# Kernel tuning notes

Measured on AMD Instinct MI355X. Metric: run time of the kernel, lower is better.

The kernel has to match this reference:

```python
import jax, jax.numpy as jnp
import numpy as np

DT = 1.0  # module init dt

def setup_inputs() -> dict:
    key = jax.random.key(0)
    k1, k2 = jax.random.split(key)
    x = jax.random.normal(k1, (8, 4096, 512), dtype=jnp.float32)
    w = jax.random.normal(k2, (512,), dtype=jnp.float32)
    return {"x": x, "w": w}

def reference(x, w):
    # h_t = h_{t-1} + dt*(x_t - relu(w)*h_{t-1}) = a*h_{t-1} + dt*x_t,  a = 1 - dt*relu(w)
    a = (1.0 - DT * jax.nn.relu(w)).astype(x.dtype)  # [d]
    h0 = jnp.zeros((x.shape[0], x.shape[2]), dtype=x.dtype)  # [b, d]
    xt = jnp.swapaxes(x, 0, 1)  # [t, b, d]

    def step(h, x_t):
        h_next = a * h + DT * x_t
        return h_next, h_next

    _, hs = jax.lax.scan(step, h0, xt)  # [t, b, d]
    return jnp.swapaxes(hs, 0, 1)  # [b, t, d] (return_sequences=True)
```

## Files before the change

kernel.cpp:

```cpp
#include <hip/hip_runtime.h>


#define RB 8
#define RT 4096
#define RD 512
#define RC 256
#define RL 16
#define DG (RD / 4)

#define HB 1e15f

__device__ __forceinline__ float sclamp(float v) {
    return fminf(fmaxf(v, -HB), HB);
}

__global__ void __launch_bounds__(DG)
k_carry(const float4* __restrict__ x4, const float4* __restrict__ w4,
        float4* __restrict__ Lc) {
    const int g  = threadIdx.x;
    const int bc = blockIdx.x;
    const int b  = bc >> 8;
    const int c  = bc & (RC - 1);

    const float4 wv = w4[g];
    const float ax = 1.0f - fmaxf(wv.x, 0.0f);
    const float ay = 1.0f - fmaxf(wv.y, 0.0f);
    const float az = 1.0f - fmaxf(wv.z, 0.0f);
    const float aw = 1.0f - fmaxf(wv.w, 0.0f);

    const float4* __restrict__ xp = x4 + ((size_t)b * RT + (size_t)c * RL) * DG + g;

    float hx = 0.f, hy = 0.f, hz = 0.f, hw = 0.f;
#pragma unroll
    for (int i = 0; i < RL; ++i) {
        const float4 v = xp[(size_t)i * DG];
        hx = sclamp(ax * hx + v.x);
        hy = sclamp(ay * hy + v.y);
        hz = sclamp(az * hz + v.z);
        hw = sclamp(aw * hw + v.w);
    }
    Lc[(size_t)bc * DG + g] = make_float4(hx, hy, hz, hw);
}

__global__ void __launch_bounds__(DG)
k_final(const float4* __restrict__ x4, const float4* __restrict__ w4,
        const float4* __restrict__ Lc, float4* __restrict__ out4) {
    const int g  = threadIdx.x;
    const int bc = blockIdx.x;
    const int b  = bc >> 8;
    const int c  = bc & (RC - 1);

    const float4 wv = w4[g];
    const float ax = 1.0f - fmaxf(wv.x, 0.0f);
    const float ay = 1.0f - fmaxf(wv.y, 0.0f);
    const float az = 1.0f - fmaxf(wv.z, 0.0f);
    const float aw = 1.0f - fmaxf(wv.w, 0.0f);

    float Ax = ax, Ay = ay, Az = az, Aw = aw;
#pragma unroll
    for (int i = 0; i < 4; ++i) {
        Ax = sclamp(Ax * Ax); Ay = sclamp(Ay * Ay);
        Az = sclamp(Az * Az); Aw = sclamp(Aw * Aw);
    }

    const float4* __restrict__ lp = Lc + (size_t)b * RC * DG + g;
    float hx = 0.f, hy = 0.f, hz = 0.f, hw = 0.f;
#pragma unroll 4
    for (int j = 0; j < c; ++j) {
        const float4 L = lp[(size_t)j * DG];
        hx = sclamp(Ax * hx + L.x);
        hy = sclamp(Ay * hy + L.y);
        hz = sclamp(Az * hz + L.z);
        hw = sclamp(Aw * hw + L.w);
    }

    const float4* __restrict__ xp = x4   + ((size_t)b * RT + (size_t)c * RL) * DG + g;
    float4*       __restrict__ op = out4 + ((size_t)b * RT + (size_t)c * RL) * DG + g;
#pragma unroll
    for (int i = 0; i < RL; ++i) {
        const float4 v = xp[(size_t)i * DG];
        hx = sclamp(ax * hx + v.x);
        hy = sclamp(ay * hy + v.y);
        hz = sclamp(az * hz + v.z);
        hw = sclamp(aw * hw + v.w);
        op[(size_t)i * DG] = make_float4(hx, hy, hz, hw);
    }
}

__global__ void __launch_bounds__(256)
rnn_seq_sat(const float* __restrict__ x, const float* __restrict__ w,
            float* __restrict__ out) {
    const int idx = blockIdx.x * blockDim.x + threadIdx.x;
    if (idx >= RB * RD) return;
    const int b = idx >> 9;
    const int d = idx & (RD - 1);
    const float a = 1.0f - fmaxf(w[d], 0.0f);
    const float* xp = x + (size_t)b * RT * RD + d;
    float* op = out + (size_t)b * RT * RD + d;
    float h = 0.f;
#pragma unroll 4
    for (int t = 0; t < RT; ++t) {
        h = sclamp(a * h + xp[(size_t)t * RD]);
        op[(size_t)t * RD] = h;
    }
}

extern "C" void kernel_launch(void* const* d_in, const int* in_sizes, int n_in,
                              void* d_out, int out_size, void* d_ws, size_t ws_size,
                              hipStream_t stream) {
    const float* x = (const float*)d_in[0];
    const float* w = (const float*)d_in[1];
    float* out = (float*)d_out;

    const size_t need = (size_t)RB * RC * DG * sizeof(float4);
    if (ws_size >= need) {
        const float4* x4 = (const float4*)x;
        const float4* w4 = (const float4*)w;
        float4* Lc = (float4*)d_ws;
        k_carry<<<dim3(RB * RC), dim3(DG), 0, stream>>>(x4, w4, Lc);
        k_final<<<dim3(RB * RC), dim3(DG), 0, stream>>>(x4, w4, Lc, (float4*)out);
    } else {
        rnn_seq_sat<<<dim3((RB * RD) / 256), dim3(256), 0, stream>>>(x, w, out);
    }
}
```

Before: 142.3 us.

## Add dedicated chunk-carry scan kernel instead of per-block quadratic prefix recompute

Each k_final block used to recompute the prefix over all previous chunk carries, which costs quadratic work and re-reads of the carries. A new k_scan kernel runs one sequential scan over the 256 chunk carries per (batch, channel group) and writes each chunk's incoming state to a second workspace buffer. k_final then loads that single state. This adds a third launch and a serial 256-step scan that uses only 16 blocks of 64 threads, and it needs twice the workspace, or else the slow fallback path runs.

```diff
diff --git a/kernel.cpp b/kernel.cpp
--- a/kernel.cpp
+++ b/kernel.cpp
@@ -42,9 +42,42 @@
     Lc[(size_t)bc * DG + g] = make_float4(hx, hy, hz, hw);
 }
 
+__global__ void __launch_bounds__(64)
+k_scan(const float4* __restrict__ w4, const float4* __restrict__ Lc,
+       float4* __restrict__ Hin) {
+    const int tid = blockIdx.x * 64 + threadIdx.x;
+    const int b = tid >> 7;
+    const int g = tid & (DG - 1);
+
+    const float4 wv = w4[g];
+    float Ax = 1.0f - fmaxf(wv.x, 0.0f);
+    float Ay = 1.0f - fmaxf(wv.y, 0.0f);
+    float Az = 1.0f - fmaxf(wv.z, 0.0f);
+    float Aw = 1.0f - fmaxf(wv.w, 0.0f);
+#pragma unroll
+    for (int i = 0; i < 4; ++i) {
+        Ax = sclamp(Ax * Ax); Ay = sclamp(Ay * Ay);
+        Az = sclamp(Az * Az); Aw = sclamp(Aw * Aw);
+    }
+
+    const float4* __restrict__ lp = Lc  + (size_t)b * RC * DG + g;
+    float4*       __restrict__ hp = Hin + (size_t)b * RC * DG + g;
+
+    float hx = 0.f, hy = 0.f, hz = 0.f, hw = 0.f;
+#pragma unroll 4
+    for (int c = 0; c < RC; ++c) {
+        hp[(size_t)c * DG] = make_float4(hx, hy, hz, hw);
+        const float4 L = lp[(size_t)c * DG];
+        hx = sclamp(Ax * hx + L.x);
+        hy = sclamp(Ay * hy + L.y);
+        hz = sclamp(Az * hz + L.z);
+        hw = sclamp(Aw * hw + L.w);
+    }
+}
+
 __global__ void __launch_bounds__(DG)
 k_final(const float4* __restrict__ x4, const float4* __restrict__ w4,
-        const float4* __restrict__ Lc, float4* __restrict__ out4) {
+        const float4* __restrict__ Hin, float4* __restrict__ out4) {
     const int g  = threadIdx.x;
     const int bc = blockIdx.x;
     const int b  = bc >> 8;
@@ -56,23 +89,8 @@
     const float az = 1.0f - fmaxf(wv.z, 0.0f);
     const float aw = 1.0f - fmaxf(wv.w, 0.0f);
 
-    float Ax = ax, Ay = ay, Az = az, Aw = aw;
-#pragma unroll
-    for (int i = 0; i < 4; ++i) {
-        Ax = sclamp(Ax * Ax); Ay = sclamp(Ay * Ay);
-        Az = sclamp(Az * Az); Aw = sclamp(Aw * Aw);
-    }
-
-    const float4* __restrict__ lp = Lc + (size_t)b * RC * DG + g;
-    float hx = 0.f, hy = 0.f, hz = 0.f, hw = 0.f;
-#pragma unroll 4
-    for (int j = 0; j < c; ++j) {
-        const float4 L = lp[(size_t)j * DG];
-        hx = sclamp(Ax * hx + L.x);
-        hy = sclamp(Ay * hy + L.y);
-        hz = sclamp(Az * hz + L.z);
-        hw = sclamp(Aw * hw + L.w);
-    }
+    const float4 H = Hin[(size_t)bc * DG + g];
+    float hx = H.x, hy = H.y, hz = H.z, hw = H.w;
 
     const float4* __restrict__ xp = x4   + ((size_t)b * RT + (size_t)c * RL) * DG + g;
     float4*       __restrict__ op = out4 + ((size_t)b * RT + (size_t)c * RL) * DG + g;
@@ -112,13 +130,15 @@
     const float* w = (const float*)d_in[1];
     float* out = (float*)d_out;
 
-    const size_t need = (size_t)RB * RC * DG * sizeof(float4);
-    if (ws_size >= need) {
+    const size_t lc_bytes = (size_t)RB * RC * DG * sizeof(float4);
+    if (ws_size >= 2 * lc_bytes) {
         const float4* x4 = (const float4*)x;
         const float4* w4 = (const float4*)w;
-        float4* Lc = (float4*)d_ws;
+        float4* Lc  = (float4*)d_ws;
+        float4* Hin = (float4*)((char*)d_ws + lc_bytes);
         k_carry<<<dim3(RB * RC), dim3(DG), 0, stream>>>(x4, w4, Lc);
-        k_final<<<dim3(RB * RC), dim3(DG), 0, stream>>>(x4, w4, Lc, (float4*)out);
+        k_scan <<<dim3((RB * DG) / 64), dim3(64), 0, stream>>>(w4, Lc, Hin);
+        k_final<<<dim3(RB * RC), dim3(DG), 0, stream>>>(x4, w4, Hin, (float4*)out);
     } else {
         rnn_seq_sat<<<dim3((RB * RD) / 256), dim3(256), 0, stream>>>(x, w, out);
     }
```

After: 154.7 us. 8.7% more time.
